# Optimization experiments

Hardware: AMD Instinct MI355X
Metric: run time of the kernel (lower is better)

The kernel has to match this reference:

```python
import jax, jax.numpy as jnp
import numpy as np
from jax import lax

TS = 64.0  # timestep_ in the original module


def get_spikes(x, th):
    # Integrate-and-fire with reset-by-subtraction (catCuda.getSpikes),
    # batched over all channels with per-channel thresholds.
    # x: [N,C,H,W,T], th: [C]
    thb = th[None, :, None, None]
    xT = jnp.moveaxis(x, -1, 0)  # [T,N,C,H,W]

    def step(v, xt):
        v = v + xt
        s = (v >= thb).astype(x.dtype)
        return v - s * thb, s

    _, sT = lax.scan(step, jnp.zeros_like(xT[0]), xT)
    return jnp.moveaxis(sT, 0, -1)  # [N,C,H,W,T]


def conv2d(x, w, b, pad):
    out = lax.conv_general_dilated(x, w, (1, 1), [(pad, pad), (pad, pad)],
                                   dimension_numbers=('NCHW', 'OIHW', 'NCHW'))
    return out + b[None, :, None, None]


def snn_conv(x, w, b, pad):
    # per-timestep 2D conv on [N,C,H,W,T]: fold T into batch
    N, C, H, W, T = x.shape
    xt = jnp.moveaxis(x, -1, 1).reshape(N * T, C, H, W)
    out = conv2d(xt, w, b, pad)
    Co, Ho, Wo = out.shape[1], out.shape[2], out.shape[3]
    return jnp.moveaxis(out.reshape(N, T, Co, Ho, Wo), 1, -1)


def avgpool2(y):
    N, C, H, W = y.shape
    return y.reshape(N, C, H // 2, 2, W // 2, 2).mean(axis=(3, 5))


def snn_pool(x):
    N, C, H, W, T = x.shape
    return x.reshape(N, C, H // 2, 2, W // 2, 2, T).mean(axis=(3, 5))


def tt(x5, y4, th):
    # threshold_training_snn: spikes from SNN pre-activation, quantized-clamped
    # ANN activation, and online per-channel threshold update.
    y_new = get_spikes(x5, th)
    y = jnp.clip(jnp.floor(y4 * TS) / TS, 0.0, 1.0)
    mul = x5.shape[0] * x5.shape[2] * x5.shape[3] * x5.shape[4]
    diff = (y.sum(axis=(0, 2, 3)) * TS - y_new.sum(axis=(0, 2, 3, 4))) / mul
    return y_new, y, th - 0.1 * diff


def setup_inputs():
    key = jax.random.key(0)
    ks = jax.random.split(key, 40)
    chans = [(3, 128), (128, 128), (128, 256), (256, 256), (256, 512), (512, 512), (512, 1024)]
    inp = {}
    for idx, (ci, co) in enumerate(chans):
        inp['w%ds' % (idx + 1)] = jax.random.normal(ks[2 * idx], (co, ci, 3, 3), jnp.float32) / np.float32(np.sqrt(ci * 9))
        inp['b%ds' % (idx + 1)] = jnp.zeros((co,), jnp.float32)
        inp['w%da' % (idx + 1)] = jax.random.normal(ks[2 * idx + 1], (co, ci, 3, 3), jnp.float32) / np.float32(np.sqrt(ci * 9))
        inp['b%da' % (idx + 1)] = jnp.zeros((co,), jnp.float32)
    inp['wc'] = jax.random.normal(ks[30], (100, 1024), jnp.float32) / 32.0
    inp['bc'] = jnp.zeros((100,), jnp.float32)
    inp['x'] = jax.random.uniform(ks[31], (4, 3, 32, 32, 64), jnp.float32)
    for name, c in [('threshold_pre_1', 128), ('threshold_pre_2', 128), ('threshold_pre_3', 256),
                    ('threshold_pre_4', 256), ('threshold_pre_5', 512), ('threshold_pre_6', 512),
                    ('threshold_pre_7', 1024), ('p1', 128), ('p2', 256), ('p3', 512), ('p4', 1024)]:
        inp[name] = jnp.ones((c,), jnp.float32)
    return inp


def reference(x, threshold_pre_1, threshold_pre_2, threshold_pre_3, threshold_pre_4,
              threshold_pre_5, threshold_pre_6, threshold_pre_7, p1, p2, p3, p4,
              w1s, b1s, w1a, b1a, w2s, b2s, w2a, b2a, w3s, b3s, w3a, b3a,
              w4s, b4s, w4a, b4a, w5s, b5s, w5a, b5a, w6s, b6s, w6a, b6a,
              w7s, b7s, w7a, b7a, wc, bc):
    x_ = x.sum(axis=-1) / TS
    xs, y, t1 = tt(snn_conv(x, w1s, b1s, 1), conv2d(x_, w1a, b1a, 1), threshold_pre_1)
    xs, y, t2 = tt(snn_conv(xs, w2s, b2s, 1), conv2d(y, w2a, b2a, 1), threshold_pre_2)
    xs, y, q1 = tt(snn_pool(xs), avgpool2(y), p1)
    xs, y, t3 = tt(snn_conv(xs, w3s, b3s, 1), conv2d(y, w3a, b3a, 1), threshold_pre_3)
    xs, y, t4 = tt(snn_conv(xs, w4s, b4s, 1), conv2d(y, w4a, b4a, 1), threshold_pre_4)
    xs, y, q2 = tt(snn_pool(xs), avgpool2(y), p2)
    xs, y, t5 = tt(snn_conv(xs, w5s, b5s, 1), conv2d(y, w5a, b5a, 1), threshold_pre_5)
    xs, y, t6 = tt(snn_conv(xs, w6s, b6s, 1), conv2d(y, w6a, b6a, 1), threshold_pre_6)
    xs, y, q3 = tt(snn_pool(xs), avgpool2(y), p3)
    xs, y, t7 = tt(snn_conv(xs, w7s, b7s, 0), conv2d(y, w7a, b7a, 0), threshold_pre_7)
    xs, y, q4 = tt(snn_pool(xs), avgpool2(y), p4)
    # classifier on [N,1024,1,1,T] spike trains, then sum over time / T
    logits_t = jnp.einsum('nct,oc->not', xs[:, :, 0, 0, :], wc) + bc[None, :, None]
    out = logits_t.sum(axis=-1) / TS
    return (out, t1, t2, t3, t4, t5, t6, t7, q1, q2, q3, q4)
```

## Files before the change

kernel.cpp:

```cpp
#include <hip/hip_runtime.h>
#include <cstdint>
#include <cstddef>


typedef short short8 __attribute__((ext_vector_type(8)));
typedef float floatx4 __attribute__((ext_vector_type(4)));

__device__ __forceinline__ unsigned short f2bf_rne(float f) {
  unsigned u = __float_as_uint(f);
  return (unsigned short)((u + 0x7FFFu + ((u >> 16) & 1u)) >> 16);
}
__device__ __forceinline__ float bf2f(unsigned short h) {
  return __uint_as_float((unsigned)h << 16);
}

__global__ __launch_bounds__(256) void k_wxform(const float* __restrict__ Wsrc,
                                                unsigned short* __restrict__ wt,
                                                int Ci, int Co) {
  const int nch = Ci >> 5;
  const int total = (Co >> 6) * nch * 9 * 4 * 64;
  int idx = blockIdx.x * 256 + threadIdx.x;
  if (idx >= total) return;
  int lane = idx & 63;
  int t2 = idx >> 6;
  int cg = t2 & 3;
  int t3 = t2 >> 2;
  int tap = t3 % 9;
  int t4 = t3 / 9;
  int ch = t4 % nch;
  int cot = t4 / nch;
  int co = cot * 64 + cg * 16 + (lane & 15);
  int cib = ch * 32 + (lane >> 4) * 8;
  short8 vh, vl;
  #pragma unroll
  for (int j = 0; j < 8; ++j) {
    float wv = Wsrc[((size_t)co * Ci + cib + j) * 9 + tap];
    unsigned short h = f2bf_rne(wv);
    vh[j] = (short)h;
    vl[j] = (short)f2bf_rne(wv - bf2f(h));
  }
  size_t base = ((((size_t)cot * nch + ch) * 9 + tap) * 4 + cg) * 1024 + (size_t)lane * 8;
  *(short8*)&wt[base] = vh;
  *(short8*)&wt[base + 512] = vl;
}

__global__ __launch_bounds__(256) void k_wxform1(const float* __restrict__ Wsrc,
                                                 unsigned short* __restrict__ wt) {
  int idx = blockIdx.x * 256 + threadIdx.x;
  if (idx >= 512) return;
  int lane = idx & 63, cg = (idx >> 6) & 3, cot = idx >> 8;
  int co = cot * 64 + cg * 16 + (lane & 15);
  short8 vh, vl;
  #pragma unroll
  for (int e = 0; e < 8; ++e) {
    int k = (lane >> 4) * 8 + e;
    float wv = 0.f;
    if (k < 27) { int tap = k / 3, ci = k - 3 * tap; wv = Wsrc[(co * 3 + ci) * 9 + tap]; }
    unsigned short h = f2bf_rne(wv);
    vh[e] = (short)h;
    vl[e] = (short)f2bf_rne(wv - bf2f(h));
  }
  size_t base = (size_t)cot * 4096 + cg * 1024 + (size_t)lane * 8;
  *(short8*)&wt[base] = vh;
  *(short8*)&wt[base + 512] = vl;
}

__global__ __launch_bounds__(256) void k_tpack(const float* __restrict__ x,
                                               unsigned* __restrict__ XT2) {
  int idx = blockIdx.x * 256 + threadIdx.x;
  int b = idx / 3072;
  int rem = idx - b * 3072;
  int t = b & 63, n = b >> 6;
  float f = x[((size_t)(n * 3072 + rem)) * 64 + t];
  unsigned short h = f2bf_rne(f);
  unsigned short l = f2bf_rne(f - bf2f(h));
  XT2[idx] = (unsigned)h | ((unsigned)l << 16);
}

__global__ __launch_bounds__(256) void k_xbar_pack(const float* __restrict__ x,
                                                   unsigned* __restrict__ xb) {
  int idx = blockIdx.x * 256 + threadIdx.x;
  if (idx >= 12288) return;
  const float* p = x + (size_t)idx * 64;
  float s = 0.f;
  #pragma unroll
  for (int t = 0; t < 64; ++t) s += p[t];
  s *= 0.015625f;
  unsigned short h = f2bf_rne(s);
  unsigned short l = f2bf_rne(s - bf2f(h));
  xb[idx] = (unsigned)h | ((unsigned)l << 16);
}

template <typename T, bool PAD0, int G>
__global__ __launch_bounds__(256, 1) void k_cmfma(
    const T* __restrict__ in, const unsigned short* __restrict__ wt,
    const float* __restrict__ bs, float* __restrict__ out,
    int Ci, int Co, int W, int TRI, int tpi, int NIMG, int nImgValid,
    int nchPer, size_t osplit) {
  constexpr int MT = 4 * G * 16;
  constexpr int PPXMAX = PAD0 ? (MT / 4) * 16 : 400;
  __shared__ unsigned short sIn[PPXMAX * 40];
  const int tid = threadIdx.x;
  const int lane = tid & 63;
  const int wv = tid >> 6;
  const int cot = blockIdx.x;
  const int mtile = blockIdx.y;
  const int kz = blockIdx.z;
  const int nch = Ci >> 5;
  const int nchA = kz * nchPer, nchB = nchA + nchPer;
  out += (size_t)kz * osplit;
  const int addBias = (kz == 0);

  int img_first, r0 = 0, PPR, PPX;
  if constexpr (PAD0) {
    img_first = mtile * (MT / 4);
    PPR = 16; PPX = (MT / 4) * 16;
  } else {
    img_first = (mtile / tpi) * NIMG;
    r0 = (mtile % tpi) * TRI;
    PPR = (TRI + 2) * (W + 2);
    PPX = NIMG * PPR;
  }
  const int TRW = TRI * W;

  int p0[G], mimg[G], mopx[G];
  #pragma unroll
  for (int g = 0; g < G; ++g) {
    int m = wv * (G * 16) + g * 16 + (lane & 15);
    int limg;
    if constexpr (PAD0) {
      limg = m >> 2;
      int o = m & 3;
      p0[g] = limg * 16 + (o >> 1) * 4 + (o & 1);
      mopx[g] = (o >> 1) * 2 + (o & 1);
    } else {
      limg = m / TRW;
      int rm = m - limg * TRW;
      int r = rm / W, c = rm - r * W;
      p0[g] = limg * PPR + r * (W + 2) + c;
      mopx[g] = (r0 + r) * W + c;
    }
    mimg[g] = img_first + limg;
  }
  int psh[9];
  #pragma unroll
  for (int t = 0; t < 9; ++t) {
    int dh = t / 3, dw = t - dh * 3;
    psh[t] = PAD0 ? (dh * 4 + dw) : (dh * (W + 2) + dw);
  }

  const int HWin = PAD0 ? 16 : W * W;
  int sgofs[2]; bool svalid[2];
  #pragma unroll
  for (int i = 0; i < 2; ++i) {
    int p = tid + i * 256;
    svalid[i] = false; sgofs[i] = 0;
    if (p < PPX) {
      int limg, gpx;
      if constexpr (PAD0) {
        limg = p >> 4; gpx = p & 15;
      } else {
        limg = p / PPR;
        int rem = p - limg * PPR;
        int pr = rem / (W + 2), pc = rem - pr * (W + 2);
        int gr = r0 + pr - 1, gc = pc - 1;
        gpx = (gr >= 0 && gr < W && gc >= 0 && gc < W) ? gr * W + gc : -1;
      }
      int img = img_first + limg;
      if (gpx >= 0 && img < nImgValid) {
        svalid[i] = true;
        sgofs[i] = img * Ci * HWin + gpx;
      }
    }
  }
  const int kb = (lane >> 4) * 8;

  floatx4 acc[4][G];
  floatx4 zero = {0.f, 0.f, 0.f, 0.f};
  #pragma unroll
  for (int cg = 0; cg < 4; ++cg)
    #pragma unroll
    for (int g = 0; g < G; ++g) acc[cg][g] = zero;

  for (int ch = nchA; ch < nchB; ++ch) {
    const int ci0 = ch * 32;
    unsigned rawu[2][32];
    float rawf[2][32];
    #pragma unroll
    for (int i = 0; i < 2; ++i) {
      if (tid + i * 256 < PPX && svalid[i]) {
        const T* sp = in + sgofs[i] + (size_t)ci0 * HWin;
        #pragma unroll
        for (int k = 0; k < 32; ++k) {
          if constexpr (sizeof(T) == 1) rawu[i][k] = sp[(size_t)k * HWin];
          else rawf[i][k] = ((const float*)sp)[(size_t)k * HWin];
        }
      }
    }
    #pragma unroll
    for (int i = 0; i < 2; ++i) {
      int p = tid + i * 256;
      if (p < PPX) {
        unsigned short* dst = &sIn[p * 40];
        if (svalid[i]) {
          #pragma unroll
          for (int j = 0; j < 4; ++j) {
            short8 v;
            #pragma unroll
            for (int e = 0; e < 8; ++e) {
              if constexpr (sizeof(T) == 1)
                v[e] = rawu[i][j * 8 + e] ? (short)0x3F80 : (short)0;
              else
                v[e] = (short)f2bf_rne(rawf[i][j * 8 + e]);
            }
            *(short8*)&dst[j * 8] = v;
          }
        } else {
          short8 z = {};
          #pragma unroll
          for (int j = 0; j < 4; ++j) *(short8*)&dst[j * 8] = z;
        }
      }
    }
    __syncthreads();
    const unsigned short* wb = wt + ((size_t)(cot * nch + ch)) * 36864 + (size_t)lane * 8;
    short8 A[2][8];
    #pragma unroll
    for (int f = 0; f < 8; ++f)
      A[0][f] = *(const short8*)(wb + (f >> 1) * 1024 + (f & 1) * 512);
    #pragma unroll
    for (int t = 0; t < 9; ++t) {
      const int cur = t & 1;
      if (t < 8) {
        #pragma unroll
        for (int f = 0; f < 8; ++f)
          A[cur ^ 1][f] = *(const short8*)(wb + (size_t)(t + 1) * 4096 + (f >> 1) * 1024 + (f & 1) * 512);
      }
      short8 b[G];
      #pragma unroll
      for (int g = 0; g < G; ++g)
        b[g] = *(const short8*)&sIn[(p0[g] + psh[t]) * 40 + kb];
      #pragma unroll
      for (int cg = 0; cg < 4; ++cg) {
        #pragma unroll
        for (int g = 0; g < G; ++g) {
          acc[cg][g] = __builtin_amdgcn_mfma_f32_16x16x32_bf16(A[cur][cg * 2 + 0], b[g], acc[cg][g], 0, 0, 0);
          acc[cg][g] = __builtin_amdgcn_mfma_f32_16x16x32_bf16(A[cur][cg * 2 + 1], b[g], acc[cg][g], 0, 0, 0);
        }
      }
    }
    __syncthreads();
  }
  const int HWout = PAD0 ? 4 : W * W;
  #pragma unroll
  for (int g = 0; g < G; ++g) {
    if (mimg[g] >= nImgValid) continue;
    #pragma unroll
    for (int cg = 0; cg < 4; ++cg) {
      #pragma unroll
      for (int i2 = 0; i2 < 4; ++i2) {
        int co = cot * 64 + cg * 16 + (lane >> 4) * 4 + i2;
        float bv = addBias ? bs[co] : 0.f;
        out[((size_t)mimg[g] * Co + co) * HWout + mopx[g]] = acc[cg][g][i2] + bv;
      }
    }
  }
}

__global__ __launch_bounds__(256, 1) void k_l1(const unsigned* __restrict__ xin,
                                               const unsigned short* __restrict__ wt,
                                               const float* __restrict__ bs,
                                               float* __restrict__ out,
                                               int nImgValid) {
  __shared__ unsigned short sIn[256 * 72];
  const int tid = threadIdx.x, lane = tid & 63, wv = tid >> 6;
  const int cot = blockIdx.x, mtile = blockIdx.y;
  const int img = mtile >> 2;
  const int r0 = (mtile & 3) * 8;
  {
    int m = tid;
    int r = r0 + (m >> 5), c = m & 31;
    const unsigned* ip = xin + (size_t)img * 3072;
    unsigned v[9][3];
    bool iv = (img < nImgValid);
    #pragma unroll
    for (int dh = 0; dh < 3; ++dh) {
      #pragma unroll
      for (int dw = 0; dw < 3; ++dw) {
        int rr = r + dh - 1, cc = c + dw - 1;
        bool ok = iv && rr >= 0 && rr < 32 && cc >= 0 && cc < 32;
        #pragma unroll
        for (int ci = 0; ci < 3; ++ci)
          v[dh * 3 + dw][ci] = ok ? ip[ci * 1024 + rr * 32 + cc] : 0u;
      }
    }
    #pragma unroll
    for (int j = 0; j < 4; ++j) {
      short8 vh, vl;
      #pragma unroll
      for (int e = 0; e < 8; ++e) {
        int k = j * 8 + e;
        unsigned u = (k < 27) ? v[k / 3][k - 3 * (k / 3)] : 0u;
        vh[e] = (short)(u & 0xFFFFu);
        vl[e] = (short)(u >> 16);
      }
      *(short8*)&sIn[m * 72 + j * 8] = vh;
      *(short8*)&sIn[m * 72 + 32 + j * 8] = vl;
    }
  }
  __syncthreads();
  const int kb = (lane >> 4) * 8;
  const unsigned short* wb = wt + (size_t)cot * 4096 + (size_t)lane * 8;
  short8 Af[8];
  #pragma unroll
  for (int f = 0; f < 8; ++f)
    Af[f] = *(const short8*)(wb + (f >> 1) * 1024 + (f & 1) * 512);
  floatx4 acc[4][4];
  floatx4 zero = {0.f, 0.f, 0.f, 0.f};
  #pragma unroll
  for (int cg = 0; cg < 4; ++cg)
    #pragma unroll
    for (int g = 0; g < 4; ++g) acc[cg][g] = zero;
  short8 bh[4], bl[4];
  #pragma unroll
  for (int g = 0; g < 4; ++g) {
    int m = wv * 64 + g * 16 + (lane & 15);
    bh[g] = *(const short8*)&sIn[m * 72 + kb];
    bl[g] = *(const short8*)&sIn[m * 72 + 32 + kb];
  }
  #pragma unroll
  for (int cg = 0; cg < 4; ++cg) {
    #pragma unroll
    for (int g = 0; g < 4; ++g) {
      acc[cg][g] = __builtin_amdgcn_mfma_f32_16x16x32_bf16(Af[cg * 2 + 0], bh[g], acc[cg][g], 0, 0, 0);
      acc[cg][g] = __builtin_amdgcn_mfma_f32_16x16x32_bf16(Af[cg * 2 + 0], bl[g], acc[cg][g], 0, 0, 0);
      acc[cg][g] = __builtin_amdgcn_mfma_f32_16x16x32_bf16(Af[cg * 2 + 1], bh[g], acc[cg][g], 0, 0, 0);
    }
  }
  if (img >= nImgValid) return;
  #pragma unroll
  for (int g = 0; g < 4; ++g) {
    int mbase = wv * 64 + g * 16 + (lane & 15);
    int px = (r0 + (mbase >> 5)) * 32 + (mbase & 31);
    #pragma unroll
    for (int cg = 0; cg < 4; ++cg) {
      #pragma unroll
      for (int i2 = 0; i2 < 4; ++i2) {
        int co = cot * 64 + cg * 16 + (lane >> 4) * 4 + i2;
        out[((size_t)img * 128 + co) * 1024 + px] = acc[cg][g][i2] + bs[co];
      }
    }
  }
}

__global__ __launch_bounds__(256) void k_pool_u8(const uint8_t* __restrict__ in,
                                                 float* __restrict__ out,
                                                 int H, int total) {
  int idx = blockIdx.x * 256 + threadIdx.x;
  if (idx >= total) return;
  int Wo = H >> 1;
  int wo = idx % Wo;
  int t1 = idx / Wo;
  int ho = t1 % Wo;
  int bc = t1 / Wo;
  size_t base = ((size_t)bc * H + 2 * ho) * H + 2 * wo;
  out[idx] = 0.25f * ((float)in[base] + (float)in[base + 1] +
                      (float)in[base + H] + (float)in[base + H + 1]);
}

__global__ __launch_bounds__(256) void k_pool_f32(const float* __restrict__ in,
                                                  float* __restrict__ out,
                                                  int H, int total) {
  int idx = blockIdx.x * 256 + threadIdx.x;
  if (idx >= total) return;
  int Wo = H >> 1;
  int wo = idx % Wo;
  int t1 = idx / Wo;
  int ho = t1 % Wo;
  int bc = t1 / Wo;
  size_t base = ((size_t)bc * H + 2 * ho) * H + 2 * wo;
  out[idx] = 0.25f * (in[base] + in[base + 1] + in[base + H] + in[base + H + 1]);
}

__global__ __launch_bounds__(256) void k_if(const float* __restrict__ X,
                                            const float* __restrict__ Xb,
                                            uint8_t* __restrict__ Sp,
                                            const float* __restrict__ th,
                                            float* __restrict__ ssum,
                                            int C, int HW) {
  const int CHW = C * HW;
  int idx = blockIdx.x * 256 + threadIdx.x;
  if (idx >= CHW) return;
  int c = idx / HW;
  const float thv = th[c];
  size_t base = (size_t)blockIdx.y * 64 * CHW + idx;
  const float* p = X + base;
  const float* pb = Xb ? (Xb + base) : nullptr;
  uint8_t* q = Sp + base;
  float v = 0.f, ss = 0.f;
  #pragma unroll
  for (int t = 0; t < 64; ++t) {
    float xv = p[(size_t)t * CHW];
    if (pb) xv += pb[(size_t)t * CHW];
    v += xv;
    float s = (v >= thv) ? 1.f : 0.f;
    v -= s * thv;
    q[(size_t)t * CHW] = (uint8_t)s;
    ss += s;
  }
  if ((HW & 63) == 0) {
    for (int off = 32; off >= 1; off >>= 1) ss += __shfl_down(ss, off);
    if ((threadIdx.x & 63) == 0) atomicAdd(&ssum[c], ss);
  } else {
    atomicAdd(&ssum[c], ss);
  }
}

__global__ __launch_bounds__(256) void k_tty(const float* __restrict__ y4,
                                             float* __restrict__ yout,
                                             float* __restrict__ ysum,
                                             int C, int HW,
                                             int nparts, int pstride) {
  int idx = blockIdx.x * 256 + threadIdx.x;
  if (idx >= 4 * C * HW) return;
  int rem = idx % (C * HW);
  int c = rem / HW;
  float xv = 0.f;
  for (int p = 0; p < nparts; ++p) xv += y4[idx + (size_t)p * pstride];
  float v = floorf(xv * 64.f) * 0.015625f;
  v = fminf(fmaxf(v, 0.f), 1.f);
  yout[idx] = v;
  if ((HW & 63) == 0) {
    for (int off = 32; off >= 1; off >>= 1) v += __shfl_down(v, off);
    if ((threadIdx.x & 63) == 0) atomicAdd(&ysum[c], v);
  } else {
    atomicAdd(&ysum[c], v);
  }
}

__global__ void k_thr(const float* __restrict__ thin,
                      const float* __restrict__ ssum,
                      const float* __restrict__ ysum,
                      float* __restrict__ dst, int C, float invmul) {
  int c = blockIdx.x * 256 + threadIdx.x;
  if (c >= C) return;
  float diff = (ysum[c] * 64.f - ssum[c]) * invmul;
  dst[c] = thin[c] - 0.1f * diff;
}

__global__ void k_sumspk(const uint8_t* __restrict__ A, float* __restrict__ S) {
  int idx = blockIdx.x * 256 + threadIdx.x;
  if (idx >= 4096) return;
  int n = idx >> 10, c = idx & 1023;
  const uint8_t* p = A + (size_t)n * 64 * 1024 + c;
  float s = 0.f;
  #pragma unroll
  for (int t = 0; t < 64; ++t) s += (float)p[t * 1024];
  S[idx] = s;
}

__global__ void k_cls(const float* __restrict__ S, const float* __restrict__ wc,
                      const float* __restrict__ bcp, float* __restrict__ out) {
  int idx = blockIdx.x * 256 + threadIdx.x;
  if (idx >= 400) return;
  int n = idx / 100, o = idx - (idx / 100) * 100;
  const float* sp = S + n * 1024;
  const float* wp = wc + o * 1024;
  float acc = 0.f;
  for (int c = 0; c < 1024; ++c) acc += wp[c] * sp[c];
  out[idx] = acc * 0.015625f + bcp[o];
}

extern "C" void kernel_launch(void* const* d_in, const int* in_sizes, int n_in,
                              void* d_out_v, int out_size, void* d_ws, size_t ws_size,
                              hipStream_t stream) {
  const float *Ws[7], *Bs[7], *Wa[7], *Ba[7];
  for (int i = 0; i < 7; ++i) {
    Ws[i] = (const float*)d_in[i * 4 + 0];
    Bs[i] = (const float*)d_in[i * 4 + 1];
    Wa[i] = (const float*)d_in[i * 4 + 2];
    Ba[i] = (const float*)d_in[i * 4 + 3];
  }
  const float* wc = (const float*)d_in[28];
  const float* bc = (const float*)d_in[29];
  const float* x  = (const float*)d_in[30];
  const float* TH[7];
  for (int i = 0; i < 7; ++i) TH[i] = (const float*)d_in[31 + i];
  const float* P[4];
  for (int i = 0; i < 4; ++i) P[i] = (const float*)d_in[38 + i];
  float* out = (float*)d_out_v;

  float* w = (float*)d_ws;
  const size_t RF = 8536064;
  float* Rb = w;
  size_t off = RF;
  float* xbar = w + off; off += 12288;
  float* yA   = w + off; off += 524288;
  float* yB   = w + off; off += 524288;
  float* y4   = w + off; off += 524288;
  float* S    = w + off; off += 4096;
  float* sums = w + off; off += 11 * 2048;
  uint8_t* SA = (uint8_t*)(w + off);
  uint8_t* SB = SA + 33554432;
  size_t total_bytes = off * sizeof(float) + (size_t)2 * 33554432;
  if (ws_size < total_bytes) return;
  unsigned short* WT = (unsigned short*)Rb;
  unsigned* XT2 = (unsigned*)SB;
  unsigned* xbar2 = (unsigned*)xbar;

  hipMemsetAsync(sums, 0, 11 * 2048 * sizeof(float), stream);
  k_tpack<<<3072, 256, 0, stream>>>(x, XT2);
  k_xbar_pack<<<48, 256, 0, stream>>>(x, xbar2);

  int stage = 0;

  {
    float* CF = Rb + 4096;
    float* ss = sums; float* ys = ss + 1024;
    k_wxform1<<<2, 256, 0, stream>>>(Ws[0], WT);
    for (int c = 0; c < 4; ++c) {
      k_l1<<<dim3(2, 256), 256, 0, stream>>>(XT2 + (size_t)c * 64 * 3072, WT, Bs[0], CF, 64);
      k_if<<<dim3(512, 1), 256, 0, stream>>>(CF, nullptr, SA + (size_t)c * 64 * 131072,
                                             TH[0], ss, 128, 1024);
    }
    k_wxform1<<<2, 256, 0, stream>>>(Wa[0], WT);
    k_l1<<<dim3(2, 16), 256, 0, stream>>>(xbar2, WT, Ba[0], y4, 4);
    k_tty<<<2048, 256, 0, stream>>>(y4, yA, ys, 128, 1024, 1, 0);
    k_thr<<<1, 256, 0, stream>>>(TH[0], ss, ys, out + 400, 128, 1.0f / (4.f * 1024.f * 64.f));
    ++stage;
  }

  auto mfma_layer = [&](const uint8_t* inS, uint8_t* outS, const float* inY, float* outY,
                        int li, int Ci, int Co, int W, int TRI, int tpi, int NIMG,
                        int chunkImgs, int kzn, float* CF1,
                        int aTRI, int atpi, int akz,
                        const float* thin, int outoff) {
    const int HW = W * W;
    const int CHWo = Co * HW;
    const int nch = Ci >> 5;
    float* ss = sums + stage * 2048; float* ys = ss + 1024;
    float* CF = Rb + (size_t)Co * Ci * 9;
    size_t osplit = (kzn == 2) ? (size_t)(CF1 - CF) : 0;
    int xgrid = ((Co / 64) * nch * 9 * 4 * 64 + 255) / 256;
    k_wxform<<<xgrid, 256, 0, stream>>>(Ws[li], WT, Ci, Co);
    int nchk = 256 / chunkImgs;
    int mt = (chunkImgs / NIMG) * tpi;
    for (int c = 0; c < nchk; ++c) {
      k_cmfma<uint8_t, false, 4><<<dim3(Co / 64, mt, kzn), 256, 0, stream>>>(
          inS + (size_t)c * chunkImgs * Ci * HW, WT, Bs[li], CF,
          Ci, Co, W, TRI, tpi, NIMG, chunkImgs, nch / kzn, osplit);
      k_if<<<dim3((CHWo + 255) / 256, chunkImgs / 64), 256, 0, stream>>>(
          CF, (kzn == 2) ? CF1 : nullptr,
          outS + (size_t)c * chunkImgs * CHWo, thin, ss, Co, HW);
    }
    k_wxform<<<xgrid, 256, 0, stream>>>(Wa[li], WT, Ci, Co);
    int aosplit = 4 * CHWo;
    k_cmfma<float, false, 1><<<dim3(Co / 64, 4 * atpi, akz), 256, 0, stream>>>(
        inY, WT, Ba[li], y4, Ci, Co, W, aTRI, atpi, 1, 4, nch / akz, (size_t)aosplit);
    k_tty<<<(4 * CHWo + 255) / 256, 256, 0, stream>>>(y4, outY, ys, Co, HW, akz, aosplit);
    k_thr<<<(Co + 255) / 256, 256, 0, stream>>>(thin, ss, ys, out + outoff, Co,
                                                1.0f / (4.f * HW * 64.f));
    ++stage;
  };

  auto pool_stage = [&](const uint8_t* inS, uint8_t* outS, const float* inY, float* outY,
                        int C, int H, const float* pthr, int outoff) {
    const int Ho = H / 2, HWo = Ho * Ho;
    const int CHWo = C * HWo;
    float* CF = Rb;
    float* ss = sums + stage * 2048; float* ys = ss + 1024;
    int tot5 = 256 * CHWo;
    k_pool_u8<<<(tot5 + 255) / 256, 256, 0, stream>>>(inS, CF, H, tot5);
    k_if<<<dim3((CHWo + 255) / 256, 4), 256, 0, stream>>>(CF, nullptr, outS, pthr, ss, C, HWo);
    int tot4 = 4 * CHWo;
    k_pool_f32<<<(tot4 + 255) / 256, 256, 0, stream>>>(inY, y4, H, tot4);
    k_tty<<<(tot4 + 255) / 256, 256, 0, stream>>>(y4, outY, ys, C, HWo, 1, 0);
    k_thr<<<(C + 255) / 256, 256, 0, stream>>>(pthr, ss, ys, out + outoff, C,
                                               1.0f / (4.f * HWo * 64.f));
    ++stage;
  };

  mfma_layer(SA, SB, yA, yB, 1, 128, 128, 32, 8, 4, 1, 64, 1, nullptr,
             2, 16, 1, TH[1], 528);
  pool_stage(SB, SA, yB, yA, 128, 32, P[0], 3216);
  mfma_layer(SA, SB, yA, yB, 2, 128, 256, 16, 16, 1, 1, 64, 2,
             (float*)(SB + 16777216), 4, 4, 2, TH[2], 656);
  mfma_layer(SB, SA, yB, yA, 3, 256, 256, 16, 16, 1, 1, 64, 2,
             (float*)(SA + 16777216), 4, 4, 2, TH[3], 912);
  pool_stage(SA, SB, yA, yB, 256, 16, P[1], 3344);
  mfma_layer(SB, SA, yB, yA, 4, 256, 512, 8, 8, 1, 4, 128, 2,
             (float*)(SA + 8388608), 8, 1, 4, TH[4], 1168);
  mfma_layer(SA, SB, yA, yB, 5, 512, 512, 8, 8, 1, 4, 128, 2,
             (float*)(SB + 8388608), 8, 1, 4, TH[5], 1680);
  pool_stage(SB, SA, yB, yA, 512, 8, P[2], 3600);
  {
    float* ss = sums + stage * 2048; float* ys = ss + 1024;
    float* CF = Rb + (size_t)1024 * 512 * 9;
    const size_t osplit = 1048576;
    int xgrid = (16 * 16 * 9 * 4 * 64 + 255) / 256;
    k_wxform<<<xgrid, 256, 0, stream>>>(Ws[6], WT, 512, 1024);
    k_cmfma<uint8_t, true, 2><<<dim3(16, 8, 2), 256, 0, stream>>>(
        SA, WT, Bs[6], CF, 512, 1024, 4, 0, 1, 0, 256, 8, osplit);
    k_if<<<dim3(16, 4), 256, 0, stream>>>(CF, CF + osplit, SB, TH[6], ss, 1024, 4);
    k_wxform<<<xgrid, 256, 0, stream>>>(Wa[6], WT, 512, 1024);
    k_cmfma<float, true, 1><<<dim3(16, 1, 8), 256, 0, stream>>>(
        yA, WT, Ba[6], y4, 512, 1024, 4, 0, 1, 0, 4, 2, 16384);
    k_tty<<<64, 256, 0, stream>>>(y4, yB, ys, 1024, 4, 8, 16384);
    k_thr<<<4, 256, 0, stream>>>(TH[6], ss, ys, out + 2192, 1024, 1.0f / 1024.f);
    ++stage;
  }
  pool_stage(SB, SA, yB, yA, 1024, 2, P[3], 4112);
  k_sumspk<<<16, 256, 0, stream>>>(SA, S);
  k_cls<<<2, 256, 0, stream>>>(S, wc, bc, out);
}
```

Measured before the change: 2.119 ms.

## Shrink SNN conv tiles, stream input loads, generalize split-K partial reduction

Drops the staged raw-register arrays in the conv MFMA kernel so each input is converted and stored to shared memory as it is loaded. This lowers register pressure, and the shared-memory size now depends on G. The SNN conv layers move from G=4 to G=2 tiles with retuned image/tile parameters. Layer 7 now splits K four ways instead of two, with its partial buffer relocated into a spike buffer. The IF kernel now sums an arbitrary number of K-split partials. The intent is higher occupancy and more blocks in flight, at the cost of less load ILP and more partial-sum traffic.

```diff
diff --git a/kernel.cpp b/kernel.cpp
--- a/kernel.cpp
+++ b/kernel.cpp
@@ -98,7 +98,7 @@
     int Ci, int Co, int W, int TRI, int tpi, int NIMG, int nImgValid,
     int nchPer, size_t osplit) {
   constexpr int MT = 4 * G * 16;
-  constexpr int PPXMAX = PAD0 ? (MT / 4) * 16 : 400;
+  constexpr int PPXMAX = PAD0 ? (MT / 4) * 16 : (G >= 4 ? 400 : 208);
   __shared__ unsigned short sIn[PPXMAX * 40];
   const int tid = threadIdx.x;
   const int lane = tid & 63;
@@ -184,34 +184,22 @@
 
   for (int ch = nchA; ch < nchB; ++ch) {
     const int ci0 = ch * 32;
-    unsigned rawu[2][32];
-    float rawf[2][32];
-    #pragma unroll
-    for (int i = 0; i < 2; ++i) {
-      if (tid + i * 256 < PPX && svalid[i]) {
-        const T* sp = in + sgofs[i] + (size_t)ci0 * HWin;
-        #pragma unroll
-        for (int k = 0; k < 32; ++k) {
-          if constexpr (sizeof(T) == 1) rawu[i][k] = sp[(size_t)k * HWin];
-          else rawf[i][k] = ((const float*)sp)[(size_t)k * HWin];
-        }
-      }
-    }
     #pragma unroll
     for (int i = 0; i < 2; ++i) {
       int p = tid + i * 256;
       if (p < PPX) {
         unsigned short* dst = &sIn[p * 40];
         if (svalid[i]) {
+          const T* sp = in + sgofs[i] + (size_t)ci0 * HWin;
           #pragma unroll
           for (int j = 0; j < 4; ++j) {
             short8 v;
             #pragma unroll
             for (int e = 0; e < 8; ++e) {
               if constexpr (sizeof(T) == 1)
-                v[e] = rawu[i][j * 8 + e] ? (short)0x3F80 : (short)0;
+                v[e] = sp[(size_t)(j * 8 + e) * HWin] ? (short)0x3F80 : (short)0;
               else
-                v[e] = (short)f2bf_rne(rawf[i][j * 8 + e]);
+                v[e] = (short)f2bf_rne(((const float*)sp)[(size_t)(j * 8 + e) * HWin]);
             }
             *(short8*)&dst[j * 8] = v;
           }
@@ -383,11 +371,11 @@
 }
 
 __global__ __launch_bounds__(256) void k_if(const float* __restrict__ X,
-                                            const float* __restrict__ Xb,
                                             uint8_t* __restrict__ Sp,
                                             const float* __restrict__ th,
                                             float* __restrict__ ssum,
-                                            int C, int HW) {
+                                            int C, int HW,
+                                            int nparts, size_t pstride) {
   const int CHW = C * HW;
   int idx = blockIdx.x * 256 + threadIdx.x;
   if (idx >= CHW) return;
@@ -395,13 +383,13 @@
   const float thv = th[c];
   size_t base = (size_t)blockIdx.y * 64 * CHW + idx;
   const float* p = X + base;
-  const float* pb = Xb ? (Xb + base) : nullptr;
   uint8_t* q = Sp + base;
   float v = 0.f, ss = 0.f;
   #pragma unroll
   for (int t = 0; t < 64; ++t) {
-    float xv = p[(size_t)t * CHW];
-    if (pb) xv += pb[(size_t)t * CHW];
+    const float* pt = p + (size_t)t * CHW;
+    float xv = pt[0];
+    for (int u = 1; u < nparts; ++u) xv += pt[(size_t)u * pstride];
     v += xv;
     float s = (v >= thv) ? 1.f : 0.f;
     v -= s * thv;
@@ -520,8 +508,8 @@
     k_wxform1<<<2, 256, 0, stream>>>(Ws[0], WT);
     for (int c = 0; c < 4; ++c) {
       k_l1<<<dim3(2, 256), 256, 0, stream>>>(XT2 + (size_t)c * 64 * 3072, WT, Bs[0], CF, 64);
-      k_if<<<dim3(512, 1), 256, 0, stream>>>(CF, nullptr, SA + (size_t)c * 64 * 131072,
-                                             TH[0], ss, 128, 1024);
+      k_if<<<dim3(512, 1), 256, 0, stream>>>(CF, SA + (size_t)c * 64 * 131072,
+                                             TH[0], ss, 128, 1024, 1, 0);
     }
     k_wxform1<<<2, 256, 0, stream>>>(Wa[0], WT);
     k_l1<<<dim3(2, 16), 256, 0, stream>>>(xbar2, WT, Ba[0], y4, 4);
@@ -546,12 +534,11 @@
     int nchk = 256 / chunkImgs;
     int mt = (chunkImgs / NIMG) * tpi;
     for (int c = 0; c < nchk; ++c) {
-      k_cmfma<uint8_t, false, 4><<<dim3(Co / 64, mt, kzn), 256, 0, stream>>>(
+      k_cmfma<uint8_t, false, 2><<<dim3(Co / 64, mt, kzn), 256, 0, stream>>>(
           inS + (size_t)c * chunkImgs * Ci * HW, WT, Bs[li], CF,
           Ci, Co, W, TRI, tpi, NIMG, chunkImgs, nch / kzn, osplit);
       k_if<<<dim3((CHWo + 255) / 256, chunkImgs / 64), 256, 0, stream>>>(
-          CF, (kzn == 2) ? CF1 : nullptr,
-          outS + (size_t)c * chunkImgs * CHWo, thin, ss, Co, HW);
+          CF, outS + (size_t)c * chunkImgs * CHWo, thin, ss, Co, HW, kzn, osplit);
     }
     k_wxform<<<xgrid, 256, 0, stream>>>(Wa[li], WT, Ci, Co);
     int aosplit = 4 * CHWo;
@@ -571,7 +558,7 @@
     float* ss = sums + stage * 2048; float* ys = ss + 1024;
     int tot5 = 256 * CHWo;
     k_pool_u8<<<(tot5 + 255) / 256, 256, 0, stream>>>(inS, CF, H, tot5);
-    k_if<<<dim3((CHWo + 255) / 256, 4), 256, 0, stream>>>(CF, nullptr, outS, pthr, ss, C, HWo);
+    k_if<<<dim3((CHWo + 255) / 256, 4), 256, 0, stream>>>(CF, outS, pthr, ss, C, HWo, 1, 0);
     int tot4 = 4 * CHWo;
     k_pool_f32<<<(tot4 + 255) / 256, 256, 0, stream>>>(inY, y4, H, tot4);
     k_tty<<<(tot4 + 255) / 256, 256, 0, stream>>>(y4, outY, ys, C, HWo, 1, 0);
@@ -580,28 +567,28 @@
     ++stage;
   };
 
-  mfma_layer(SA, SB, yA, yB, 1, 128, 128, 32, 8, 4, 1, 64, 1, nullptr,
+  mfma_layer(SA, SB, yA, yB, 1, 128, 128, 32, 4, 8, 1, 64, 1, nullptr,
              2, 16, 1, TH[1], 528);
   pool_stage(SB, SA, yB, yA, 128, 32, P[0], 3216);
-  mfma_layer(SA, SB, yA, yB, 2, 128, 256, 16, 16, 1, 1, 64, 2,
+  mfma_layer(SA, SB, yA, yB, 2, 128, 256, 16, 8, 2, 1, 64, 2,
              (float*)(SB + 16777216), 4, 4, 2, TH[2], 656);
-  mfma_layer(SB, SA, yB, yA, 3, 256, 256, 16, 16, 1, 1, 64, 2,
+  mfma_layer(SB, SA, yB, yA, 3, 256, 256, 16, 8, 2, 1, 64, 2,
              (float*)(SA + 16777216), 4, 4, 2, TH[3], 912);
   pool_stage(SA, SB, yA, yB, 256, 16, P[1], 3344);
-  mfma_layer(SB, SA, yB, yA, 4, 256, 512, 8, 8, 1, 4, 128, 2,
+  mfma_layer(SB, SA, yB, yA, 4, 256, 512, 8, 8, 1, 2, 128, 2,
              (float*)(SA + 8388608), 8, 1, 4, TH[4], 1168);
-  mfma_layer(SA, SB, yA, yB, 5, 512, 512, 8, 8, 1, 4, 128, 2,
+  mfma_layer(SA, SB, yA, yB, 5, 512, 512, 8, 8, 1, 2, 128, 2,
              (float*)(SB + 8388608), 8, 1, 4, TH[5], 1680);
   pool_stage(SB, SA, yB, yA, 512, 8, P[2], 3600);
   {
     float* ss = sums + stage * 2048; float* ys = ss + 1024;
-    float* CF = Rb + (size_t)1024 * 512 * 9;
+    float* CF = (float*)(SA + 4194304);
     const size_t osplit = 1048576;
     int xgrid = (16 * 16 * 9 * 4 * 64 + 255) / 256;
     k_wxform<<<xgrid, 256, 0, stream>>>(Ws[6], WT, 512, 1024);
-    k_cmfma<uint8_t, true, 2><<<dim3(16, 8, 2), 256, 0, stream>>>(
-        SA, WT, Bs[6], CF, 512, 1024, 4, 0, 1, 0, 256, 8, osplit);
-    k_if<<<dim3(16, 4), 256, 0, stream>>>(CF, CF + osplit, SB, TH[6], ss, 1024, 4);
+    k_cmfma<uint8_t, true, 2><<<dim3(16, 8, 4), 256, 0, stream>>>(
+        SA, WT, Bs[6], CF, 512, 1024, 4, 0, 1, 0, 256, 4, osplit);
+    k_if<<<dim3(16, 4), 256, 0, stream>>>(CF, SB, TH[6], ss, 1024, 4, 4, osplit);
     k_wxform<<<xgrid, 256, 0, stream>>>(Wa[6], WT, 512, 1024);
     k_cmfma<float, true, 1><<<dim3(16, 1, 8), 256, 0, stream>>>(
         yA, WT, Ba[6], y4, 512, 1024, 4, 0, 1, 0, 4, 2, 16384);
```

Measured after the change: 1.974 ms. -6.9%, faster.
